# Kernel tuning notes

Measured on AMD Instinct MI355X. Metric: run time of the kernel, lower is better.

Reference implementation:

```python
import jax, jax.numpy as jnp
import numpy as np

N_LENGTH = 64
MAX_NUM_FRAME = 16
EPS = 1e-6  # torch pairwise_distance eps


def setup_inputs() -> dict:
    key = jax.random.key(0)
    x = jax.random.normal(key, (8, N_LENGTH, 3, 224, 224), dtype=jnp.float32)
    # frozen conv params per init_parameters(): weight=0.001, bias=0
    conv_w = jnp.full((1, 3, 7, 7), 0.001, dtype=jnp.float32)
    conv_b = jnp.zeros((1,), dtype=jnp.float32)
    return {"x": x, "conv_w": conv_w, "conv_b": conv_b}


def reference(x, conv_w, conv_b):
    B, L, C, H, W = x.shape
    xc = x.reshape(B * L, C, H, W)
    # shallow_conv: 3->1 channels, 7x7, stride 1, pad 3
    y = jax.lax.conv_general_dilated(
        xc, conv_w, window_strides=(1, 1), padding=[(3, 3), (3, 3)],
        dimension_numbers=("NCHW", "OIHW", "NCHW"))
    y = y + conv_b[None, :, None, None]
    y = y.reshape(B, L, H * W)  # out channels == 1, flattened spatially

    # PairwiseDistance(p=2) over the singleton channel dim: |a - b + eps|
    pa = jnp.abs(y[:, :-1, :] - y[:, 1:, :] + EPS)  # (B, L-1, H*W)

    diff_score = pa.sum(axis=-1)  # (B, L-1) == PA.sum(dim=(-2,-1))
    ratio = MAX_NUM_FRAME / N_LENGTH
    dsp = jnp.power(diff_score, ratio ** 0.5)
    frac = dsp / dsp.sum(axis=-1, keepdims=True)
    # einsum('bl,ml->bml', frac, tril_ones).sum(-1) is a cumsum along l
    cum = jnp.cumsum(frac, axis=-1)  # (B, L-1)

    interval = 1.0 / (MAX_NUM_FRAME - 1)
    sample = jnp.arange(MAX_NUM_FRAME, dtype=jnp.float32) * interval  # (M,)
    # vectorized argmin over all M sample points at once
    idx = jnp.argmin(jnp.abs(cum[:, None, :] - sample[None, :, None]), axis=-1)  # (B, M)

    sel = jnp.take_along_axis(x, idx[:, :, None, None, None], axis=1)  # (B, M, 3, H, W)
    return sel
```

## Files before the change

kernel.cpp:

```cpp
#include <hip/hip_runtime.h>
#include <float.h>
#include <math.h>

#define HH 224
#define WW 224
#define PLANE (HH*WW)
#define FRAME (3*HH*WW)
#define LFR 64
#define NP 63
#define NB 8
#define NM 16
#define EPSV 1e-6f

#define RSLAB 32
#define NSLAB (HH / RSLAB)
#define DROWS (RSLAB + 6)

__global__ __launch_bounds__(256) void diff_kernel(
    const float* __restrict__ x, const float* __restrict__ cw,
    float* __restrict__ dsp)
{
    const int slab = blockIdx.x;
    const int pair = blockIdx.y;
    const int b = pair / NP;
    const int l = pair - b * NP;
    const float* f0 = x + (size_t)(b * LFR + l) * FRAME;
    const float* f1 = f0 + FRAME;
    const float w = cw[0];

    const int i0 = slab * RSLAB;
    const int rBase = i0 - 3;

    __shared__ float Vbuf[RSLAB][WW];

    const int tid = threadIdx.x;
    const bool act = tid < WW;
    float acc = 0.f;

    if (act) {
        float d[DROWS];
        #pragma unroll
        for (int k = 0; k < DROWS; ++k) {
            const int r = rBase + k;
            float v = 0.f;
            if (r >= 0 && r < HH) {
                const int off = r * WW + tid;
                v = (f0[off]           - f1[off])
                  + (f0[PLANE + off]   - f1[PLANE + off])
                  + (f0[2*PLANE + off] - f1[2*PLANE + off]);
            }
            d[k] = v;
        }
        #pragma unroll
        for (int ko = 0; ko < RSLAB; ++ko) {
            float v = d[ko] + d[ko+1] + d[ko+2] + d[ko+3]
                    + d[ko+4] + d[ko+5] + d[ko+6];
            Vbuf[ko][tid] = v;
        }
    }
    __syncthreads();

    if (act) {
        #pragma unroll 4
        for (int ko = 0; ko < RSLAB; ++ko) {
            float s = 0.f;
            #pragma unroll
            for (int dj = -3; dj <= 3; ++dj) {
                const int j = tid + dj;
                if (j >= 0 && j < WW) s += Vbuf[ko][j];
            }
            acc += fabsf(w * s + EPSV);
        }
    }

    #pragma unroll
    for (int off = 32; off >= 1; off >>= 1)
        acc += __shfl_down(acc, off, 64);
    __shared__ float red[4];
    const int wave = tid >> 6;
    if ((tid & 63) == 0) red[wave] = acc;
    __syncthreads();
    if (tid == 0)
        dsp[pair * NSLAB + slab] = red[0] + red[1] + red[2] + red[3];
}

__global__ __launch_bounds__(64) void select_kernel(
    const float* __restrict__ dsp, int* __restrict__ idx)
{
    const int b = blockIdx.x;
    const int lane = threadIdx.x;
    float v = 0.f;
    if (lane < NP) {
        float s = 0.f;
        #pragma unroll
        for (int k = 0; k < NSLAB; ++k) s += dsp[(b * NP + lane) * NSLAB + k];
        v = sqrtf(s);
    }

    float tot = v;
    #pragma unroll
    for (int off = 1; off < 64; off <<= 1)
        tot += __shfl_xor(tot, off, 64);

    float scan = v;
    #pragma unroll
    for (int off = 1; off < 64; off <<= 1) {
        float t = __shfl_up(scan, off, 64);
        if (lane >= off) scan += t;
    }
    const float cum = scan / tot;

    const float interval = 1.0f / (NM - 1);
    for (int m = 0; m < NM; ++m) {
        const float target = (float)m * interval;
        float bv = (lane < NP) ? fabsf(cum - target) : FLT_MAX;
        int bi = lane;
        #pragma unroll
        for (int off = 1; off < 64; off <<= 1) {
            float ov = __shfl_xor(bv, off, 64);
            int oi = __shfl_xor(bi, off, 64);
            if (ov < bv || (ov == bv && oi < bi)) { bv = ov; bi = oi; }
        }
        if (lane == 0) idx[b * NM + m] = bi;
    }
}

__global__ __launch_bounds__(256) void gather_kernel(
    const float* __restrict__ x, const int* __restrict__ idx,
    float* __restrict__ out)
{
    const int f = blockIdx.y;
    const int b = f >> 4;
    const int id = idx[f];
    const float4* src = (const float4*)(x + (size_t)(b * LFR + id) * FRAME);
    float4* dst = (float4*)(out + (size_t)f * FRAME);
    const int i = blockIdx.x * 256 + threadIdx.x;
    #pragma unroll
    for (int k = 0; k < 7; ++k)
        dst[i + k * (21 * 256)] = src[i + k * (21 * 256)];
}

extern "C" void kernel_launch(void* const* d_in, const int* in_sizes, int n_in,
                              void* d_out, int out_size, void* d_ws, size_t ws_size,
                              hipStream_t stream) {
    const float* x  = (const float*)d_in[0];
    const float* cw = (const float*)d_in[1];
    float* dsp = (float*)d_ws;
    int*   idx = (int*)((char*)d_ws + 16384);

    hipLaunchKernelGGL(diff_kernel, dim3(NSLAB, NB * NP), dim3(256), 0, stream,
                       x, cw, dsp);
    hipLaunchKernelGGL(select_kernel, dim3(NB), dim3(64), 0, stream, dsp, idx);
    hipLaunchKernelGGL(gather_kernel, dim3(21, NB * NM), dim3(256), 0, stream,
                       x, idx, (float*)d_out);
}
```

Baseline: 500.5 us.

## Load channel-summed frame diffs with float4 into padded LDS, then separable box filter

```diff
diff --git a/kernel.cpp b/kernel.cpp
--- a/kernel.cpp
+++ b/kernel.cpp
@@ -15,6 +15,9 @@
 #define RSLAB 32
 #define NSLAB (HH / RSLAB)
 #define DROWS (RSLAB + 6)
+#define LDW 232
+#define NQ 56
+#define UNITS (DROWS * NQ)
 
 __global__ __launch_bounds__(256) void diff_kernel(
     const float* __restrict__ x, const float* __restrict__ cw,
@@ -28,55 +31,65 @@
     const float* f1 = f0 + FRAME;
     const float w = cw[0];
 
-    const int i0 = slab * RSLAB;
-    const int rBase = i0 - 3;
+    const int rBase = slab * RSLAB - 3;
 
-    __shared__ float Vbuf[RSLAB][WW];
+    __shared__ float Dl[DROWS][LDW];
+    __shared__ float red[4];
 
     const int tid = threadIdx.x;
-    const bool act = tid < WW;
-    float acc = 0.f;
 
-    if (act) {
-        float d[DROWS];
-        #pragma unroll
-        for (int k = 0; k < DROWS; ++k) {
-            const int r = rBase + k;
-            float v = 0.f;
-            if (r >= 0 && r < HH) {
-                const int off = r * WW + tid;
-                v = (f0[off]           - f1[off])
-                  + (f0[PLANE + off]   - f1[PLANE + off])
-                  + (f0[2*PLANE + off] - f1[2*PLANE + off]);
-            }
-            d[k] = v;
+    if (tid < 2 * DROWS) {
+        const int r = tid >> 1;
+        const int col = (tid & 1) ? (LDW - 4) : 0;
+        *(float4*)&Dl[r][col] = make_float4(0.f, 0.f, 0.f, 0.f);
+    }
+
+    for (int u = tid; u < UNITS; u += 256) {
+        const int r  = u / NQ;
+        const int cq = u - r * NQ;
+        const int gr = rBase + r;
+        float4 v = make_float4(0.f, 0.f, 0.f, 0.f);
+        if (gr >= 0 && gr < HH) {
+            const int off = (gr * WW + cq * 4) >> 2;
+            const float4* p0 = (const float4*)f0;
+            const float4* p1 = (const float4*)f1;
+            const float4 a0 = p0[off];
+            const float4 a1 = p0[off + PLANE/4];
+            const float4 a2 = p0[off + 2*PLANE/4];
+            const float4 b0 = p1[off];
+            const float4 b1 = p1[off + PLANE/4];
+            const float4 b2 = p1[off + 2*PLANE/4];
+            v.x = (a0.x - b0.x) + (a1.x - b1.x) + (a2.x - b2.x);
+            v.y = (a0.y - b0.y) + (a1.y - b1.y) + (a2.y - b2.y);
+            v.z = (a0.z - b0.z) + (a1.z - b1.z) + (a2.z - b2.z);
+            v.w = (a0.w - b0.w) + (a1.w - b1.w) + (a2.w - b2.w);
         }
-        #pragma unroll
-        for (int ko = 0; ko < RSLAB; ++ko) {
-            float v = d[ko] + d[ko+1] + d[ko+2] + d[ko+3]
-                    + d[ko+4] + d[ko+5] + d[ko+6];
-            Vbuf[ko][tid] = v;
-        }
+        *(float4*)&Dl[r][4 + cq * 4] = v;
     }
     __syncthreads();
 
-    if (act) {
-        #pragma unroll 4
-        for (int ko = 0; ko < RSLAB; ++ko) {
-            float s = 0.f;
+    float acc = 0.f;
+    if (tid < WW) {
+        const int base = 4 + tid;
+        float hring[8];
+        #pragma unroll
+        for (int r = 0; r < DROWS; ++r) {
+            float h = 0.f;
             #pragma unroll
-            for (int dj = -3; dj <= 3; ++dj) {
-                const int j = tid + dj;
-                if (j >= 0 && j < WW) s += Vbuf[ko][j];
+            for (int k = 0; k < 7; ++k) h += Dl[r][base - 3 + k];
+            hring[r & 7] = h;
+            if (r >= 6) {
+                float v = 0.f;
+                #pragma unroll
+                for (int k = 0; k < 7; ++k) v += hring[(r - 6 + k) & 7];
+                acc += fabsf(w * v + EPSV);
             }
-            acc += fabsf(w * s + EPSV);
         }
     }
 
     #pragma unroll
     for (int off = 32; off >= 1; off >>= 1)
         acc += __shfl_down(acc, off, 64);
-    __shared__ float red[4];
     const int wave = tid >> 6;
     if ((tid & 63) == 0) red[wave] = acc;
     __syncthreads();
```

Result: faster. 467.2 us (-6.6%).
